# Performance work log

Hardware: AMD Instinct MI355X
Metric: run time of the kernel (lower is better)

The kernel has to match this reference:

```python
import jax, jax.numpy as jnp
import numpy as np

N, E, G, F = 100000, 3200000, 256, 15
NEG_SLOPE = 0.2


def _lin(k, fi, fo):
    s = 1.0 / np.sqrt(fi)
    return jax.random.uniform(k, (fi, fo), jnp.float32, -s, s)


def _vec(k, n, fi):
    s = 1.0 / np.sqrt(fi)
    return jax.random.uniform(k, (n,), jnp.float32, -s, s)


def setup_inputs() -> dict:
    key = jax.random.key(0)
    ks = jax.random.split(key, 40)
    inp = {}
    inp["x"] = jax.random.normal(ks[0], (N, F), jnp.float32)
    inp["edge_index"] = jax.random.randint(ks[1], (2, E), 0, N, dtype=jnp.int32)
    inp["batch"] = jnp.sort(jax.random.randint(ks[2], (N,), 0, G, dtype=jnp.int32))
    inp["xA"] = jax.random.normal(ks[3], (G, 300), jnp.float32)
    i = 4
    for l in (1, 2, 3):
        inp[f"cW{l}"] = _lin(ks[i], F, F); i += 1
        inp[f"cas{l}"] = _vec(ks[i], F, F); i += 1
        inp[f"cad{l}"] = _vec(ks[i], F, F); i += 1
        inp[f"cb{l}"] = jnp.zeros((F,), jnp.float32)
        inp[f"fW{l}"] = _lin(ks[i], F, F); i += 1
        inp[f"fb{l}"] = _vec(ks[i], F, F); i += 1
    inp["m1W"] = _lin(ks[i], 90, 90); i += 1
    inp["m1b"] = _vec(ks[i], 90, 90); i += 1
    inp["aW1"] = _lin(ks[i], 300, 300); i += 1
    inp["ab1"] = _vec(ks[i], 300, 300); i += 1
    inp["aW2"] = _lin(ks[i], 300, 300); i += 1
    inp["ab2"] = _vec(ks[i], 300, 300); i += 1
    inp["aW3"] = _lin(ks[i], 300, 300); i += 1
    inp["ab3"] = _vec(ks[i], 300, 300); i += 1
    inp["aW4"] = _lin(ks[i], 300, 45); i += 1
    inp["ab4"] = _vec(ks[i], 45, 300); i += 1
    inp["m2W"] = _lin(ks[i], 90, 1); i += 1
    inp["m2b"] = _vec(ks[i], 1, 90); i += 1
    return inp


def _gat(x, src, dst, W, a_s, a_d, b):
    """PyG GATConv (heads=1, add_self_loops handled by caller via src/dst)."""
    h = x @ W                                        # [N, F]
    e = jax.nn.leaky_relu((h @ a_s)[src] + (h @ a_d)[dst], NEG_SLOPE)  # [E+N]
    mx = jax.ops.segment_max(e, dst, num_segments=N)
    ex = jnp.exp(e - mx[dst])
    den = jax.ops.segment_sum(ex, dst, num_segments=N)
    alpha = ex / (den[dst] + 1e-16)                   # segment softmax over dst
    out = jax.ops.segment_sum(h[src] * alpha[:, None], dst, num_segments=N)
    return out + b


def reference(x, edge_index, batch, xA,
              cW1, cas1, cad1, cb1, fW1, fb1,
              cW2, cas2, cad2, cb2, fW2, fb2,
              cW3, cas3, cad3, cb3, fW3, fb3,
              m1W, m1b, aW1, ab1, aW2, ab2, aW3, ab3, aW4, ab4,
              m2W, m2b):
    loop = jnp.arange(N, dtype=edge_index.dtype)      # self loops
    src = jnp.concatenate([edge_index[0], loop])
    dst = jnp.concatenate([edge_index[1], loop])

    h = _gat(x, src, dst, cW1, cas1, cad1, cb1)
    h = jax.nn.relu(h @ fW1 + fb1)
    h = _gat(h, src, dst, cW2, cas2, cad2, cb2)
    h = jax.nn.relu(h @ fW2 + fb2)
    h = _gat(h, src, dst, cW3, cas3, cad3, cb3)
    h = h @ fW3 + fb3

    s = jax.ops.segment_sum(h, batch, num_segments=G)
    mx = jax.ops.segment_max(h, batch, num_segments=G)
    cnt = jax.ops.segment_sum(jnp.ones((N, 1), h.dtype), batch, num_segments=G)
    mean = s / jnp.maximum(cnt, 1.0)
    pooled = jnp.concatenate([s, mx, mean], axis=1)   # [G, 45]

    a = jax.nn.relu(xA @ aW1 + ab1)
    a = jax.nn.relu(a @ aW2 + ab2)
    a = jax.nn.sigmoid(a @ aW3 + ab3)
    xann = a @ aW4 + ab4                              # [G, 45]

    z = jnp.concatenate([pooled, xann], axis=1)       # [G, 90]
    z = jax.nn.relu(z @ m1W + m1b)
    z = z @ m2W + m2b
    return jax.nn.sigmoid(z)
```

## Files before the change

### kernel.cpp

```cpp
#include <hip/hip_runtime.h>
#include <hip/hip_bf16.h>
#include <math.h>

#define FDIM 15
#define FPAD 16
#define NEG_SLOPE 0.2f
#define BSH 8
#define BWID 256
#define HB_GRID 256
#define HB_BLK 1024

typedef _Float16 half_t;

__device__ __forceinline__ float leaky(float e) {
  return fmaxf(NEG_SLOPE * e, e);
}

__global__ void k_zero(int* __restrict__ p, int n) {
  int i = blockIdx.x * blockDim.x + threadIdx.x;
  if (i < n) p[i] = 0;
}

__global__ void k_bhist(const int* __restrict__ dstI, int* __restrict__ bcnt,
                        int n_tot, int n_real, int NB) {
  __shared__ int hist[512];
  int tid = threadIdx.x;
  for (int i = tid; i < NB; i += blockDim.x) hist[i] = 0;
  __syncthreads();
  int stride = gridDim.x * blockDim.x;
  for (int i = blockIdx.x * blockDim.x + tid; i < n_tot; i += stride) {
    int d = (i < n_real) ? dstI[i] : (i - n_real);
    atomicAdd(&hist[d >> BSH], 1);
  }
  __syncthreads();
  for (int i = tid; i < NB; i += blockDim.x)
    if (hist[i]) atomicAdd(&bcnt[i], hist[i]);
}

__global__ void k_bscan(const int* __restrict__ bcnt, int* __restrict__ boff,
                        int* __restrict__ bcur, int* __restrict__ rowptr,
                        int NB, int N, int total) {
  __shared__ int s[512];
  int tid = threadIdx.x;
  int v = (tid < NB) ? bcnt[tid] : 0;
  s[tid] = v;
  __syncthreads();
  for (int off = 1; off < 512; off <<= 1) {
    int add = (tid >= off) ? s[tid - off] : 0;
    __syncthreads();
    s[tid] += add;
    __syncthreads();
  }
  if (tid < NB) { int e = s[tid] - v; boff[tid] = e; bcur[tid] = e; }
  if (tid == NB - 1) boff[NB] = s[tid];
  if (tid == 0) rowptr[N] = total;
}

__global__ void k_bpart(const int* __restrict__ srcI, const int* __restrict__ dstI,
                        int* __restrict__ bcur, int* __restrict__ bbuf,
                        int n_tot, int n_real, int NB) {
  __shared__ int hist[512];
  __shared__ int base[512];
  int tid = threadIdx.x;
  for (int i = tid; i < NB; i += blockDim.x) hist[i] = 0;
  __syncthreads();
  int stride = gridDim.x * blockDim.x;
  int g0 = blockIdx.x * blockDim.x + tid;
  for (int i = g0; i < n_tot; i += stride) {
    int d = (i < n_real) ? dstI[i] : (i - n_real);
    atomicAdd(&hist[d >> BSH], 1);
  }
  __syncthreads();
  for (int i = tid; i < NB; i += blockDim.x)
    base[i] = hist[i] ? atomicAdd(&bcur[i], hist[i]) : 0;
  __syncthreads();
  for (int i = tid; i < NB; i += blockDim.x) hist[i] = 0;
  __syncthreads();
  for (int i = g0; i < n_tot; i += stride) {
    int s, d;
    if (i < n_real) { s = srcI[i]; d = dstI[i]; }
    else { s = d = i - n_real; }
    int b = d >> BSH;
    int p = base[b] + atomicAdd(&hist[b], 1);
    bbuf[p] = (s << BSH) | (d & (BWID - 1));
  }
}

__global__ void k_bbuild(const int* __restrict__ boff, const int* __restrict__ bbuf,
                         int* __restrict__ rowptr, int* __restrict__ csr, int N) {
  __shared__ int hist[BWID];
  __shared__ int sc[BWID];
  int b = blockIdx.x;
  int tid = threadIdx.x;
  int base_dst = b << BSH;
  int nd = min(BWID, N - base_dst);
  int s0 = boff[b], s1 = boff[b + 1];
  if (tid < BWID) hist[tid] = 0;
  __syncthreads();
  for (int j = s0 + tid; j < s1; j += 512)
    atomicAdd(&hist[bbuf[j] & (BWID - 1)], 1);
  __syncthreads();
  int v = 0;
  if (tid < BWID) { v = hist[tid]; sc[tid] = v; }
  __syncthreads();
  for (int off = 1; off < BWID; off <<= 1) {
    int add = 0;
    if (tid < BWID && tid >= off) add = sc[tid - off];
    __syncthreads();
    if (tid < BWID) sc[tid] += add;
    __syncthreads();
  }
  if (tid < nd) rowptr[base_dst + tid] = s0 + sc[tid] - v;
  __syncthreads();
  if (tid < BWID) hist[tid] = sc[tid] - v;
  __syncthreads();
  for (int j = s0 + tid; j < s1; j += 512) {
    int e = bbuf[j];
    int dl = e & (BWID - 1);
    int p = s0 + atomicAdd(&hist[dl], 1);
    csr[p] = (e >> BSH) << 5;
  }
}

__global__ void k_transform(const float* __restrict__ in, int ld_in,
                            const float* __restrict__ W,
                            const float* __restrict__ a_s,
                            const float* __restrict__ a_d,
                            half_t* __restrict__ hp,
                            float* __restrict__ ad_,
                            int n_nodes) {
  __shared__ float Ws[FDIM * FDIM];
  __shared__ float asv[FDIM], adv[FDIM];
  int tid = threadIdx.x;
  if (tid < FDIM * FDIM) Ws[tid] = W[tid];
  if (tid < FDIM) { asv[tid] = a_s[tid]; adv[tid] = a_d[tid]; }
  __syncthreads();
  int n = blockIdx.x * blockDim.x + tid;
  if (n >= n_nodes) return;
  float xin[FDIM];
#pragma unroll
  for (int j = 0; j < FDIM; ++j) xin[j] = in[n * ld_in + j];
  float sa = 0.f, da = 0.f;
  half_t hrow[FPAD];
#pragma unroll
  for (int o = 0; o < FDIM; ++o) {
    float acc = 0.f;
#pragma unroll
    for (int k = 0; k < FDIM; ++k) acc += xin[k] * Ws[k * FDIM + o];
    hrow[o] = (half_t)acc;
    sa += acc * asv[o];
    da += acc * adv[o];
  }
  hrow[FDIM] = (half_t)sa;
  ad_[n] = da;
  float4 w0, w1;
  __builtin_memcpy(&w0, &hrow[0], 16);
  __builtin_memcpy(&w1, &hrow[8], 16);
  float4* dst = (float4*)(hp + (size_t)n * FPAD);
  dst[0] = w0;
  dst[1] = w1;
}

__device__ __forceinline__ void mlp_rider(int g, int tid, int nthreads,
                                          const float* __restrict__ mIn,
                                          const float* __restrict__ mW,
                                          const float* __restrict__ mB,
                                          float* __restrict__ mOut,
                                          int Nout, int mAct,
                                          float* mins) {
  for (int k = tid; k < 300; k += nthreads) mins[k] = mIn[(size_t)g * 300 + k];
  __syncthreads();
  int j1 = tid;
  int j2 = tid + nthreads;
  bool p1 = (j1 < Nout), p2 = (j2 < Nout);
  if (!p1) return;
  float a0 = 0.f, a1 = 0.f, a2 = 0.f, a3 = 0.f;
  float a4 = 0.f, a5 = 0.f, a6 = 0.f, a7 = 0.f;
  float b0 = 0.f, b1 = 0.f, b2 = 0.f, b3 = 0.f;
  float b4 = 0.f, b5 = 0.f, b6 = 0.f, b7 = 0.f;
  int k = 0;
  for (; k + 7 < 300; k += 8) {
    float i0 = mins[k],     i1 = mins[k + 1], i2 = mins[k + 2], i3 = mins[k + 3];
    float i4 = mins[k + 4], i5 = mins[k + 5], i6 = mins[k + 6], i7 = mins[k + 7];
    float w0 = mW[k * Nout + j1];
    float w1 = mW[(k + 1) * Nout + j1];
    float w2 = mW[(k + 2) * Nout + j1];
    float w3 = mW[(k + 3) * Nout + j1];
    float w4 = mW[(k + 4) * Nout + j1];
    float w5 = mW[(k + 5) * Nout + j1];
    float w6 = mW[(k + 6) * Nout + j1];
    float w7 = mW[(k + 7) * Nout + j1];
    a0 += i0 * w0; a1 += i1 * w1; a2 += i2 * w2; a3 += i3 * w3;
    a4 += i4 * w4; a5 += i5 * w5; a6 += i6 * w6; a7 += i7 * w7;
    if (p2) {
      float v0 = mW[k * Nout + j2];
      float v1 = mW[(k + 1) * Nout + j2];
      float v2 = mW[(k + 2) * Nout + j2];
      float v3 = mW[(k + 3) * Nout + j2];
      float v4 = mW[(k + 4) * Nout + j2];
      float v5 = mW[(k + 5) * Nout + j2];
      float v6 = mW[(k + 6) * Nout + j2];
      float v7 = mW[(k + 7) * Nout + j2];
      b0 += i0 * v0; b1 += i1 * v1; b2 += i2 * v2; b3 += i3 * v3;
      b4 += i4 * v4; b5 += i5 * v5; b6 += i6 * v6; b7 += i7 * v7;
    }
  }
  for (; k < 300; ++k) {
    float ik = mins[k];
    a0 += ik * mW[k * Nout + j1];
    if (p2) b0 += ik * mW[k * Nout + j2];
  }
  float r1 = mB[j1] + ((a0 + a1) + (a2 + a3)) + ((a4 + a5) + (a6 + a7));
  if (mAct == 1) r1 = fmaxf(r1, 0.f);
  else if (mAct == 2) r1 = 1.f / (1.f + expf(-r1));
  mOut[(size_t)g * Nout + j1] = r1;
  if (p2) {
    float r2 = mB[j2] + ((b0 + b1) + (b2 + b3)) + ((b4 + b5) + (b6 + b7));
    if (mAct == 1) r2 = fmaxf(r2, 0.f);
    else if (mAct == 2) r2 = 1.f / (1.f + expf(-r2));
    mOut[(size_t)g * Nout + j2] = r2;
  }
}

__global__ void k_gat(const int* __restrict__ rowptr, const int* __restrict__ csrB,
                      const half_t* __restrict__ hp, const float* __restrict__ ad_,
                      const float* __restrict__ cb, const float* __restrict__ fW,
                      const float* __restrict__ fb,
                      const float* __restrict__ nW, const float* __restrict__ nas,
                      const float* __restrict__ nad,
                      half_t* __restrict__ hp2, float* __restrict__ ad2,
                      float* __restrict__ fout,
                      const float* __restrict__ mIn, const float* __restrict__ mW,
                      const float* __restrict__ mB, float* __restrict__ mOut,
                      int mNout, int mAct, int mlpG,
                      int n_nodes, int do_relu, int fuse) {
  __shared__ float Ws[FDIM * FDIM];
  __shared__ float W2s[FDIM * FDIM];
  __shared__ float cbv[FDIM], fbv[FDIM], as2v[FDIM], ad2v[FDIM];
  __shared__ float aggT[16][16];
  __shared__ float outT[16][16];
  __shared__ float mins[304];
  int tid = threadIdx.x;

  if ((int)blockIdx.x < mlpG) {
    mlp_rider(blockIdx.x, tid, blockDim.x, mIn, mW, mB, mOut, mNout, mAct, mins);
    return;
  }

  if (tid < FDIM * FDIM) Ws[tid] = fW[tid];
  if (tid < FDIM) { cbv[tid] = cb[tid]; fbv[tid] = fb[tid]; }
  if (fuse) {
    if (tid < FDIM * FDIM) W2s[tid] = nW[tid];
    if (tid < FDIM) { as2v[tid] = nas[tid]; ad2v[tid] = nad[tid]; }
  }
  __syncthreads();
  int dl = tid >> 4;
  int f  = tid & 15;
  int d  = ((int)blockIdx.x - mlpG) * 16 + dl;
  float val = 0.f;
  if (d < n_nodes) {
    int rs = rowptr[d], re = rowptr[d + 1];
    float adv = ad_[d];
    const char* hb = (const char*)hp;
    int fo = f << 1;
    float den0 = 0.f, acc0 = 0.f, den1 = 0.f, acc1 = 0.f;
    int j = rs;
    for (; j + 7 < re; j += 8) {
      int o0 = csrB[j],     o1 = csrB[j + 1], o2 = csrB[j + 2], o3 = csrB[j + 3];
      int o4 = csrB[j + 4], o5 = csrB[j + 5], o6 = csrB[j + 6], o7 = csrB[j + 7];
      float hv0 = (float)*(const half_t*)(hb + o0 + fo);
      float hv1 = (float)*(const half_t*)(hb + o1 + fo);
      float hv2 = (float)*(const half_t*)(hb + o2 + fo);
      float hv3 = (float)*(const half_t*)(hb + o3 + fo);
      float hv4 = (float)*(const half_t*)(hb + o4 + fo);
      float hv5 = (float)*(const half_t*)(hb + o5 + fo);
      float hv6 = (float)*(const half_t*)(hb + o6 + fo);
      float hv7 = (float)*(const half_t*)(hb + o7 + fo);
      float w0 = __expf(leaky(__shfl(hv0, 15, 16) + adv));
      float w1 = __expf(leaky(__shfl(hv1, 15, 16) + adv));
      float w2 = __expf(leaky(__shfl(hv2, 15, 16) + adv));
      float w3 = __expf(leaky(__shfl(hv3, 15, 16) + adv));
      float w4 = __expf(leaky(__shfl(hv4, 15, 16) + adv));
      float w5 = __expf(leaky(__shfl(hv5, 15, 16) + adv));
      float w6 = __expf(leaky(__shfl(hv6, 15, 16) + adv));
      float w7 = __expf(leaky(__shfl(hv7, 15, 16) + adv));
      den0 += w0; acc0 += hv0 * w0;
      den1 += w1; acc1 += hv1 * w1;
      den0 += w2; acc0 += hv2 * w2;
      den1 += w3; acc1 += hv3 * w3;
      den0 += w4; acc0 += hv4 * w4;
      den1 += w5; acc1 += hv5 * w5;
      den0 += w6; acc0 += hv6 * w6;
      den1 += w7; acc1 += hv7 * w7;
    }
    for (; j < re; ++j) {
      int o0 = csrB[j];
      float hv0 = (float)*(const half_t*)(hb + o0 + fo);
      float w0 = __expf(leaky(__shfl(hv0, 15, 16) + adv));
      den0 += w0; acc0 += hv0 * w0;
    }
    val = (acc0 + acc1) / (den0 + den1 + 1e-16f);
  }
  aggT[dl][f] = (f < FDIM) ? (val + cbv[f]) : 0.f;
  __syncthreads();
  int o = f;
  float ffn = 0.f;
  if (o < FDIM) {
    ffn = fbv[o];
#pragma unroll
    for (int k = 0; k < FDIM; ++k) ffn += aggT[dl][k] * Ws[k * FDIM + o];
    if (do_relu) ffn = fmaxf(ffn, 0.f);
  }
  if (!fuse) {
    if (d < n_nodes) fout[d * FPAD + o] = (o < FDIM) ? ffn : 0.f;
    return;
  }
  outT[dl][o] = ffn;
  __syncthreads();
  if (d < n_nodes) {
    float h2 = 0.f;
    if (o < FDIM) {
#pragma unroll
      for (int k = 0; k < FDIM; ++k) h2 += outT[dl][k] * W2s[k * FDIM + o];
    }
    float pa = (o < FDIM) ? h2 * as2v[o] : 0.f;
    float pd = (o < FDIM) ? h2 * ad2v[o] : 0.f;
#pragma unroll
    for (int k = 8; k; k >>= 1) {
      pa += __shfl_xor(pa, k, 16);
      pd += __shfl_xor(pd, k, 16);
    }
    hp2[(size_t)d * FPAD + o] = (half_t)((o < FDIM) ? h2 : pa);
    if (o == 0) ad2[d] = pd;
  }
}

__device__ __forceinline__ int lowerb(const int* __restrict__ a, int n, int key) {
  int lo = 0, hi = n;
  while (lo < hi) { int mid = (lo + hi) >> 1; if (a[mid] < key) lo = mid + 1; else hi = mid; }
  return lo;
}

__global__ void k_pool(const float* __restrict__ fout, const int* __restrict__ batch,
                       float* __restrict__ pooled,
                       const float* __restrict__ acts,
                       const float* __restrict__ aW4, const float* __restrict__ ab4,
                       float* __restrict__ xann,
                       int n_nodes, int Gn) {
  __shared__ float ss[256], sm[256];
  __shared__ float mins[304];
  int tid = threadIdx.x;
  if ((int)blockIdx.x < Gn) {
    mlp_rider(blockIdx.x, tid, blockDim.x, acts, aW4, ab4, xann, 45, 0, mins);
    return;
  }
  int g = blockIdx.x - Gn;
  int s = lowerb(batch, n_nodes, g);
  int e = lowerb(batch, n_nodes, g + 1);
  int f = tid & 15;
  float sum = 0.f, mx = -INFINITY;
  for (int n = s + (tid >> 4); n < e; n += 16) {
    float v = fout[n * FPAD + f];
    sum += v;
    mx = fmaxf(mx, v);
  }
  ss[tid] = sum; sm[tid] = mx;
  __syncthreads();
  for (int step = 128; step >= 16; step >>= 1) {
    if (tid < step) { ss[tid] += ss[tid + step]; sm[tid] = fmaxf(sm[tid], sm[tid + step]); }
    __syncthreads();
  }
  if (tid < FDIM) {
    float cnt = (float)(e - s);
    float sv = ss[tid];
    pooled[g * 45 + tid] = sv;
    pooled[g * 45 + 15 + tid] = sm[tid];
    pooled[g * 45 + 30 + tid] = sv / fmaxf(cnt, 1.f);
  }
}

__global__ void k_final(const float* __restrict__ pooled, const float* __restrict__ xann,
                        const float* __restrict__ m1W, const float* __restrict__ m1b,
                        const float* __restrict__ m2W, const float* __restrict__ m2b,
                        float* __restrict__ out) {
  __shared__ float z[90];
  __shared__ float z2[90];
  __shared__ float ps[128];
  int g = blockIdx.x;
  int t = threadIdx.x;
  if (t < 45) z[t] = pooled[g * 45 + t];
  else if (t < 90) z[t] = xann[g * 45 + (t - 45)];
  __syncthreads();
  if (t < 90) {
    float a0 = 0.f, a1 = 0.f;
    for (int k = 0; k < 90; k += 2) {
      float w0 = m1W[k * 90 + t];
      float w1 = m1W[(k + 1) * 90 + t];
      a0 += z[k] * w0; a1 += z[k + 1] * w1;
    }
    z2[t] = fmaxf(m1b[t] + a0 + a1, 0.f);
  }
  __syncthreads();
  if (t < 90) ps[t] = z2[t] * m2W[t];
  else ps[t] = 0.f;
  __syncthreads();
  if (t < 64) {
    float v = ps[t] + ps[t + 64];
#pragma unroll
    for (int k2 = 32; k2; k2 >>= 1) v += __shfl_xor(v, k2, 64);
    if (t == 0) out[g] = 1.f / (1.f + expf(-(v + m2b[0])));
  }
}

extern "C" void kernel_launch(void* const* d_in, const int* in_sizes, int n_in,
                              void* d_out, int out_size, void* d_ws, size_t ws_size,
                              hipStream_t stream) {
  const float* x   = (const float*)d_in[0];
  const int* ei    = (const int*)d_in[1];
  const int* batch = (const int*)d_in[2];
  const float* xA  = (const float*)d_in[3];

  const int N = in_sizes[0] / FDIM;
  const int E = in_sizes[1] / 2;
  const int G = in_sizes[3] / 300;
  const int ET = E + N;
  const int NB = (N + BWID - 1) >> BSH;

  const int* srcI = ei;
  const int* dstI = ei + E;

  float* ws = (float*)d_ws;
  size_t layerW = (size_t)34 * N;
  size_t uSize = layerW > (size_t)ET ? layerW : (size_t)ET;
  size_t off = 0;
  int*    bbuf = (int*)(ws + off);
  half_t* hpA  = (half_t*)(ws + off);
  half_t* hpB  = (half_t*)(ws + off + (size_t)8 * N);
  float*  adA  = ws + off + (size_t)16 * N;
  float*  adB  = ws + off + (size_t)17 * N;
  float*  fout = ws + off + (size_t)18 * N;
  off += uSize;
  int*   rowptr = (int*)(ws + off); off += N + 1;
  int*   csr    = (int*)(ws + off); off += (size_t)ET;
  int*   bcnt   = (int*)(ws + off); off += 516;
  int*   boff   = (int*)(ws + off); off += 516;
  int*   bcur   = (int*)(ws + off); off += 516;
  float* pooled = ws + off; off += (size_t)G * 45;
  float* a1     = ws + off; off += (size_t)G * 300;
  float* a2     = ws + off; off += (size_t)G * 300;
  float* xann   = ws + off; off += (size_t)G * 45;

  const int B = 256;
  const int gN = (N + B - 1) / B;

  k_zero<<<(NB + B - 1) / B, B, 0, stream>>>(bcnt, NB);
  k_bhist<<<HB_GRID, HB_BLK, 0, stream>>>(dstI, bcnt, ET, E, NB);
  k_bscan<<<1, 512, 0, stream>>>(bcnt, boff, bcur, rowptr, NB, N, ET);
  k_bpart<<<HB_GRID, HB_BLK, 0, stream>>>(srcI, dstI, bcur, bbuf, ET, E, NB);
  k_bbuild<<<NB, 512, 0, stream>>>(boff, bbuf, rowptr, csr, N);

  const float* cW1  = (const float*)d_in[4];
  const float* cas1 = (const float*)d_in[5];
  const float* cad1 = (const float*)d_in[6];
  const float* cb1  = (const float*)d_in[7];
  const float* fW1  = (const float*)d_in[8];
  const float* fb1  = (const float*)d_in[9];
  const float* cW2  = (const float*)d_in[10];
  const float* cas2 = (const float*)d_in[11];
  const float* cad2 = (const float*)d_in[12];
  const float* cb2  = (const float*)d_in[13];
  const float* fW2  = (const float*)d_in[14];
  const float* fb2  = (const float*)d_in[15];
  const float* cW3  = (const float*)d_in[16];
  const float* cas3 = (const float*)d_in[17];
  const float* cad3 = (const float*)d_in[18];
  const float* cb3  = (const float*)d_in[19];
  const float* fW3  = (const float*)d_in[20];
  const float* fb3  = (const float*)d_in[21];
  const float* m1W  = (const float*)d_in[22];
  const float* m1b  = (const float*)d_in[23];
  const float* aW1  = (const float*)d_in[24];
  const float* ab1  = (const float*)d_in[25];
  const float* aW2  = (const float*)d_in[26];
  const float* ab2  = (const float*)d_in[27];
  const float* aW3  = (const float*)d_in[28];
  const float* ab3  = (const float*)d_in[29];
  const float* aW4  = (const float*)d_in[30];
  const float* ab4  = (const float*)d_in[31];
  const float* m2W  = (const float*)d_in[32];
  const float* m2b  = (const float*)d_in[33];

  const int gGat = (N + 15) / 16;
  k_transform<<<gN, B, 0, stream>>>(x, FDIM, cW1, cas1, cad1, hpA, adA, N);
  k_gat<<<gGat + G, B, 0, stream>>>(rowptr, csr, hpA, adA, cb1, fW1, fb1,
                                    cW2, cas2, cad2, hpB, adB, nullptr,
                                    xA, aW1, ab1, a1, 300, 1, G,
                                    N, 1, 1);
  k_gat<<<gGat + G, B, 0, stream>>>(rowptr, csr, hpB, adB, cb2, fW2, fb2,
                                    cW3, cas3, cad3, hpA, adA, nullptr,
                                    a1, aW2, ab2, a2, 300, 1, G,
                                    N, 1, 1);
  k_gat<<<gGat + G, B, 0, stream>>>(rowptr, csr, hpA, adA, cb3, fW3, fb3,
                                    nullptr, nullptr, nullptr, nullptr, nullptr, fout,
                                    a2, aW3, ab3, a1, 300, 2, G,
                                    N, 0, 0);

  k_pool<<<2 * G, B, 0, stream>>>(fout, batch, pooled, a1, aW4, ab4, xann, N, G);

  k_final<<<G, 128, 0, stream>>>(pooled, xann, m1W, m1b, m2W, m2b, (float*)d_out);
}
```

Measured before the change: 361.3 us.

## Gather four halves per lane and process four edges per sub-group in GAT aggregation

Restructures the per-destination aggregation so each 16-lane group handles four edges at a time, with each lane loading 8 bytes (four fp16 features) instead of a single half. Partial sums are reduced across edge slots using xor shuffles. This cuts the number of gather instructions and the per-edge exp/shuffle work per lane. The cost is padding waste on short rows, since clamped indices still issue loads, plus an extra cross-lane reduction at the end.

New measurement: 335.1 us. 1.08x faster.

```diff
diff --git a/kernel.cpp b/kernel.cpp
--- a/kernel.cpp
+++ b/kernel.cpp
@@ -256,52 +256,59 @@
   __syncthreads();
   int dl = tid >> 4;
   int f  = tid & 15;
+  int e4 = f >> 2;
+  int c  = f & 3;
   int d  = ((int)blockIdx.x - mlpG) * 16 + dl;
-  float val = 0.f;
+  float r0 = 0.f, r1 = 0.f, r2 = 0.f, r3 = 0.f;
   if (d < n_nodes) {
     int rs = rowptr[d], re = rowptr[d + 1];
     float adv = ad_[d];
     const char* hb = (const char*)hp;
-    int fo = f << 1;
-    float den0 = 0.f, acc0 = 0.f, den1 = 0.f, acc1 = 0.f;
-    int j = rs;
-    for (; j + 7 < re; j += 8) {
-      int o0 = csrB[j],     o1 = csrB[j + 1], o2 = csrB[j + 2], o3 = csrB[j + 3];
-      int o4 = csrB[j + 4], o5 = csrB[j + 5], o6 = csrB[j + 6], o7 = csrB[j + 7];
-      float hv0 = (float)*(const half_t*)(hb + o0 + fo);
-      float hv1 = (float)*(const half_t*)(hb + o1 + fo);
-      float hv2 = (float)*(const half_t*)(hb + o2 + fo);
-      float hv3 = (float)*(const half_t*)(hb + o3 + fo);
-      float hv4 = (float)*(const half_t*)(hb + o4 + fo);
-      float hv5 = (float)*(const half_t*)(hb + o5 + fo);
-      float hv6 = (float)*(const half_t*)(hb + o6 + fo);
-      float hv7 = (float)*(const half_t*)(hb + o7 + fo);
-      float w0 = __expf(leaky(__shfl(hv0, 15, 16) + adv));
-      float w1 = __expf(leaky(__shfl(hv1, 15, 16) + adv));
-      float w2 = __expf(leaky(__shfl(hv2, 15, 16) + adv));
-      float w3 = __expf(leaky(__shfl(hv3, 15, 16) + adv));
-      float w4 = __expf(leaky(__shfl(hv4, 15, 16) + adv));
-      float w5 = __expf(leaky(__shfl(hv5, 15, 16) + adv));
-      float w6 = __expf(leaky(__shfl(hv6, 15, 16) + adv));
-      float w7 = __expf(leaky(__shfl(hv7, 15, 16) + adv));
-      den0 += w0; acc0 += hv0 * w0;
-      den1 += w1; acc1 += hv1 * w1;
-      den0 += w2; acc0 += hv2 * w2;
-      den1 += w3; acc1 += hv3 * w3;
-      den0 += w4; acc0 += hv4 * w4;
-      den1 += w5; acc1 += hv5 * w5;
-      den0 += w6; acc0 += hv6 * w6;
-      den1 += w7; acc1 += hv7 * w7;
+    int co = c << 3;
+    int srcl = f | 3;
+    float acc0 = 0.f, acc1 = 0.f, acc2 = 0.f, acc3 = 0.f, den = 0.f;
+    for (int j = rs; j < re; j += 8) {
+      int i0 = j + e4;
+      int i1 = i0 + 4;
+      int o0 = csrB[i0 < re ? i0 : re - 1];
+      int o1 = csrB[i1 < re ? i1 : re - 1];
+      uint2 u0 = *(const uint2*)(hb + o0 + co);
+      uint2 u1 = *(const uint2*)(hb + o1 + co);
+      half_t h0[4], h1[4];
+      __builtin_memcpy(h0, &u0, 8);
+      __builtin_memcpy(h1, &u1, 8);
+      float a0 = (float)h0[0], a1 = (float)h0[1], a2 = (float)h0[2], a3 = (float)h0[3];
+      float b0 = (float)h1[0], b1 = (float)h1[1], b2 = (float)h1[2], b3 = (float)h1[3];
+      float s0 = __shfl(a3, srcl, 16);
+      float s1 = __shfl(b3, srcl, 16);
+      float w0 = (i0 < re) ? __expf(leaky(s0 + adv)) : 0.f;
+      float w1 = (i1 < re) ? __expf(leaky(s1 + adv)) : 0.f;
+      den  += w0 + w1;
+      acc0 += a0 * w0 + b0 * w1;
+      acc1 += a1 * w0 + b1 * w1;
+      acc2 += a2 * w0 + b2 * w1;
+      acc3 += a3 * w0 + b3 * w1;
     }
-    for (; j < re; ++j) {
-      int o0 = csrB[j];
-      float hv0 = (float)*(const half_t*)(hb + o0 + fo);
-      float w0 = __expf(leaky(__shfl(hv0, 15, 16) + adv));
-      den0 += w0; acc0 += hv0 * w0;
-    }
-    val = (acc0 + acc1) / (den0 + den1 + 1e-16f);
-  }
-  aggT[dl][f] = (f < FDIM) ? (val + cbv[f]) : 0.f;
+    den  += __shfl_xor(den,  4, 16);
+    acc0 += __shfl_xor(acc0, 4, 16);
+    acc1 += __shfl_xor(acc1, 4, 16);
+    acc2 += __shfl_xor(acc2, 4, 16);
+    acc3 += __shfl_xor(acc3, 4, 16);
+    den  += __shfl_xor(den,  8, 16);
+    acc0 += __shfl_xor(acc0, 8, 16);
+    acc1 += __shfl_xor(acc1, 8, 16);
+    acc2 += __shfl_xor(acc2, 8, 16);
+    acc3 += __shfl_xor(acc3, 8, 16);
+    float inv = 1.f / (den + 1e-16f);
+    r0 = acc0 * inv; r1 = acc1 * inv; r2 = acc2 * inv; r3 = acc3 * inv;
+  }
+  if (e4 == 0) {
+    int base = c << 2;
+    aggT[dl][base]     = r0 + cbv[base];
+    aggT[dl][base + 1] = r1 + cbv[base + 1];
+    aggT[dl][base + 2] = r2 + cbv[base + 2];
+    aggT[dl][base + 3] = (base + 3 < FDIM) ? (r3 + cbv[base + 3]) : 0.f;
+  }
   __syncthreads();
   int o = f;
   float ffn = 0.f;
```

## Reuse per-block histograms in partition and vectorize GAT edge gather per lane

Applied to the files above, without the earlier changes.

k_bhist now saves each block's bucket histogram to global memory, so k_bpart no longer re-reads dst indices to rebuild it and skips one pass over the edge list. The GAT aggregation changes from one feature per lane with a scalar half load per edge to one edge per lane: each lane loads the full 32-byte padded row with two uint4 loads, software-prefetched two edges ahead, and accumulates all 16 channels. A shuffle transpose-reduce then combines the lanes, and the softmax normalization and conv bias are folded into the following FFN matmul through a precomputed cb·W term. This cuts the number of memory transactions per edge, at the cost of more registers and a shuffle reduction per node.

After: 321.5 us. 11.0% less time.

```diff
diff --git a/kernel.cpp b/kernel.cpp
--- a/kernel.cpp
+++ b/kernel.cpp
@@ -22,6 +22,7 @@
 }
 
 __global__ void k_bhist(const int* __restrict__ dstI, int* __restrict__ bcnt,
+                        int* __restrict__ bhistG,
                         int n_tot, int n_real, int NB) {
   __shared__ int hist[512];
   int tid = threadIdx.x;
@@ -33,8 +34,11 @@
     atomicAdd(&hist[d >> BSH], 1);
   }
   __syncthreads();
-  for (int i = tid; i < NB; i += blockDim.x)
-    if (hist[i]) atomicAdd(&bcnt[i], hist[i]);
+  for (int i = tid; i < NB; i += blockDim.x) {
+    int h = hist[i];
+    bhistG[blockIdx.x * 512 + i] = h;
+    if (h) atomicAdd(&bcnt[i], h);
+  }
 }
 
 __global__ void k_bscan(const int* __restrict__ bcnt, int* __restrict__ boff,
@@ -58,24 +62,19 @@
 
 __global__ void k_bpart(const int* __restrict__ srcI, const int* __restrict__ dstI,
                         int* __restrict__ bcur, int* __restrict__ bbuf,
+                        const int* __restrict__ bhistG,
                         int n_tot, int n_real, int NB) {
   __shared__ int hist[512];
   __shared__ int base[512];
   int tid = threadIdx.x;
-  for (int i = tid; i < NB; i += blockDim.x) hist[i] = 0;
+  for (int i = tid; i < NB; i += blockDim.x) {
+    int h = bhistG[blockIdx.x * 512 + i];
+    base[i] = h ? atomicAdd(&bcur[i], h) : 0;
+    hist[i] = 0;
+  }
   __syncthreads();
   int stride = gridDim.x * blockDim.x;
   int g0 = blockIdx.x * blockDim.x + tid;
-  for (int i = g0; i < n_tot; i += stride) {
-    int d = (i < n_real) ? dstI[i] : (i - n_real);
-    atomicAdd(&hist[d >> BSH], 1);
-  }
-  __syncthreads();
-  for (int i = tid; i < NB; i += blockDim.x)
-    base[i] = hist[i] ? atomicAdd(&bcur[i], hist[i]) : 0;
-  __syncthreads();
-  for (int i = tid; i < NB; i += blockDim.x) hist[i] = 0;
-  __syncthreads();
   for (int i = g0; i < n_tot; i += stride) {
     int s, d;
     if (i < n_real) { s = srcI[i]; d = dstI[i]; }
@@ -237,6 +236,7 @@
   __shared__ float Ws[FDIM * FDIM];
   __shared__ float W2s[FDIM * FDIM];
   __shared__ float cbv[FDIM], fbv[FDIM], as2v[FDIM], ad2v[FDIM];
+  __shared__ float cbW[16];
   __shared__ float aggT[16][16];
   __shared__ float outT[16][16];
   __shared__ float mins[304];
@@ -254,61 +254,90 @@
     if (tid < FDIM) { as2v[tid] = nas[tid]; ad2v[tid] = nad[tid]; }
   }
   __syncthreads();
+  if (tid < 16) {
+    float s = 0.f;
+    if (tid < FDIM) {
+#pragma unroll
+      for (int k = 0; k < FDIM; ++k) s += cbv[k] * Ws[k * FDIM + tid];
+    }
+    cbW[tid] = s;
+  }
   int dl = tid >> 4;
   int f  = tid & 15;
   int d  = ((int)blockIdx.x - mlpG) * 16 + dl;
-  float val = 0.f;
   if (d < n_nodes) {
     int rs = rowptr[d], re = rowptr[d + 1];
+    int rlast = re - 1;
     float adv = ad_[d];
     const char* hb = (const char*)hp;
-    int fo = f << 1;
-    float den0 = 0.f, acc0 = 0.f, den1 = 0.f, acc1 = 0.f;
-    int j = rs;
-    for (; j + 7 < re; j += 8) {
-      int o0 = csrB[j],     o1 = csrB[j + 1], o2 = csrB[j + 2], o3 = csrB[j + 3];
-      int o4 = csrB[j + 4], o5 = csrB[j + 5], o6 = csrB[j + 6], o7 = csrB[j + 7];
-      float hv0 = (float)*(const half_t*)(hb + o0 + fo);
-      float hv1 = (float)*(const half_t*)(hb + o1 + fo);
-      float hv2 = (float)*(const half_t*)(hb + o2 + fo);
-      float hv3 = (float)*(const half_t*)(hb + o3 + fo);
-      float hv4 = (float)*(const half_t*)(hb + o4 + fo);
-      float hv5 = (float)*(const half_t*)(hb + o5 + fo);
-      float hv6 = (float)*(const half_t*)(hb + o6 + fo);
-      float hv7 = (float)*(const half_t*)(hb + o7 + fo);
-      float w0 = __expf(leaky(__shfl(hv0, 15, 16) + adv));
-      float w1 = __expf(leaky(__shfl(hv1, 15, 16) + adv));
-      float w2 = __expf(leaky(__shfl(hv2, 15, 16) + adv));
-      float w3 = __expf(leaky(__shfl(hv3, 15, 16) + adv));
-      float w4 = __expf(leaky(__shfl(hv4, 15, 16) + adv));
-      float w5 = __expf(leaky(__shfl(hv5, 15, 16) + adv));
-      float w6 = __expf(leaky(__shfl(hv6, 15, 16) + adv));
-      float w7 = __expf(leaky(__shfl(hv7, 15, 16) + adv));
-      den0 += w0; acc0 += hv0 * w0;
-      den1 += w1; acc1 += hv1 * w1;
-      den0 += w2; acc0 += hv2 * w2;
-      den1 += w3; acc1 += hv3 * w3;
-      den0 += w4; acc0 += hv4 * w4;
-      den1 += w5; acc1 += hv5 * w5;
-      den0 += w6; acc0 += hv6 * w6;
-      den1 += w7; acc1 += hv7 * w7;
-    }
-    for (; j < re; ++j) {
-      int o0 = csrB[j];
-      float hv0 = (float)*(const half_t*)(hb + o0 + fo);
-      float w0 = __expf(leaky(__shfl(hv0, 15, 16) + adv));
-      den0 += w0; acc0 += hv0 * w0;
-    }
-    val = (acc0 + acc1) / (den0 + den1 + 1e-16f);
-  }
-  aggT[dl][f] = (f < FDIM) ? (val + cbv[f]) : 0.f;
+    float acc[16];
+#pragma unroll
+    for (int k = 0; k < 16; ++k) acc[k] = 0.f;
+
+    int i0 = rs + f;
+    int oA = csrB[i0 < re ? i0 : rlast];
+    uint4 aLo = *(const uint4*)(hb + oA);
+    uint4 aHi = *(const uint4*)(hb + oA + 16);
+    int i1 = i0 + 16;
+    int oB = csrB[i1 < re ? i1 : rlast];
+
+    for (int j = rs; j < re; j += 16) {
+      uint4 bLo = *(const uint4*)(hb + oB);
+      uint4 bHi = *(const uint4*)(hb + oB + 16);
+      int i2 = j + 32 + f;
+      int oC = csrB[i2 < re ? i2 : rlast];
+      half_t hv[16];
+      __builtin_memcpy(hv, &aLo, 16);
+      __builtin_memcpy(hv + 8, &aHi, 16);
+      float sa = (float)hv[15];
+      float w = (j + f < re) ? __expf(leaky(sa + adv)) : 0.f;
+#pragma unroll
+      for (int k = 0; k < FDIM; ++k) acc[k] += w * (float)hv[k];
+      acc[15] += w;
+      aLo = bLo; aHi = bHi; oB = oC;
+    }
+
+    {
+      bool hi = (f & 1);
+#pragma unroll
+      for (int i = 0; i < 8; ++i) {
+        float send = hi ? acc[i] : acc[8 + i];
+        float got = __shfl_xor(send, 1, 16);
+        acc[i] = (hi ? acc[8 + i] : acc[i]) + got;
+      }
+      hi = (f & 2);
+#pragma unroll
+      for (int i = 0; i < 4; ++i) {
+        float send = hi ? acc[i] : acc[4 + i];
+        float got = __shfl_xor(send, 2, 16);
+        acc[i] = (hi ? acc[4 + i] : acc[i]) + got;
+      }
+      hi = (f & 4);
+#pragma unroll
+      for (int i = 0; i < 2; ++i) {
+        float send = hi ? acc[i] : acc[2 + i];
+        float got = __shfl_xor(send, 4, 16);
+        acc[i] = (hi ? acc[2 + i] : acc[i]) + got;
+      }
+      hi = (f & 8);
+      {
+        float send = hi ? acc[0] : acc[1];
+        float got = __shfl_xor(send, 8, 16);
+        acc[0] = (hi ? acc[1] : acc[0]) + got;
+      }
+    }
+    int fb = ((f & 1) << 3) | ((f & 2) << 1) | ((f & 4) >> 1) | ((f & 8) >> 3);
+    aggT[dl][fb] = acc[0];
+  }
   __syncthreads();
   int o = f;
   float ffn = 0.f;
-  if (o < FDIM) {
-    ffn = fbv[o];
-#pragma unroll
-    for (int k = 0; k < FDIM; ++k) ffn += aggT[dl][k] * Ws[k * FDIM + o];
+  if (o < FDIM && d < n_nodes) {
+    float inv = 1.f / (aggT[dl][15] + 1e-16f);
+    float s = 0.f;
+#pragma unroll
+    for (int k = 0; k < FDIM; ++k) s += aggT[dl][k] * Ws[k * FDIM + o];
+    ffn = fbv[o] + cbW[o] + s * inv;
     if (do_relu) ffn = fmaxf(ffn, 0.f);
   }
   if (!fuse) {
@@ -445,6 +474,7 @@
   int*   bcnt   = (int*)(ws + off); off += 516;
   int*   boff   = (int*)(ws + off); off += 516;
   int*   bcur   = (int*)(ws + off); off += 516;
+  int*   bhistG = (int*)(ws + off); off += (size_t)512 * HB_GRID;
   float* pooled = ws + off; off += (size_t)G * 45;
   float* a1     = ws + off; off += (size_t)G * 300;
   float* a2     = ws + off; off += (size_t)G * 300;
@@ -454,9 +484,9 @@
   const int gN = (N + B - 1) / B;
 
   k_zero<<<(NB + B - 1) / B, B, 0, stream>>>(bcnt, NB);
-  k_bhist<<<HB_GRID, HB_BLK, 0, stream>>>(dstI, bcnt, ET, E, NB);
+  k_bhist<<<HB_GRID, HB_BLK, 0, stream>>>(dstI, bcnt, bhistG, ET, E, NB);
   k_bscan<<<1, 512, 0, stream>>>(bcnt, boff, bcur, rowptr, NB, N, ET);
-  k_bpart<<<HB_GRID, HB_BLK, 0, stream>>>(srcI, dstI, bcur, bbuf, ET, E, NB);
+  k_bpart<<<HB_GRID, HB_BLK, 0, stream>>>(srcI, dstI, bcur, bbuf, bhistG, ET, E, NB);
   k_bbuild<<<NB, 512, 0, stream>>>(boff, bbuf, rowptr, csr, N);
 
   const float* cW1  = (const float*)d_in[4];
```
